# Kernel tuning notes

Hardware: AMD Instinct MI355X
Metric: run time of the kernel (lower is better)

Reference implementation:

```python
import jax, jax.numpy as jnp
import numpy as np

N = 50000      # nodes
E = 800000     # edges (avg degree 16)
NE = 100000    # query edges
IN = 128; HID = 128; OUT = 128; FEAT = 2


def _linear_params(k, fan_in, fan_out):
    # torch.nn.Linear default init: U(-1/sqrt(fan_in), 1/sqrt(fan_in))
    s = 1.0 / np.sqrt(fan_in)
    k1, k2 = jax.random.split(k)
    W = jax.random.uniform(k1, (fan_in, fan_out), jnp.float32, -s, s)
    b = jax.random.uniform(k2, (fan_out,), jnp.float32, -s, s)
    return W, b


def setup_inputs() -> dict:
    key = jax.random.key(0)
    ks = jax.random.split(key, 9)
    inp = {}
    inp["x"] = jax.random.normal(ks[0], (N, IN), jnp.float32)
    inp["adj_t"] = jax.random.randint(ks[1], (2, E), 0, N)          # edge_index [2,E]
    inp["train_edges"] = jax.random.randint(ks[2], (NE, 2), 0, N)   # query edges
    # GCNConv stack params (lin weight + bias per layer)
    inp["W1"], inp["b1"] = _linear_params(ks[3], IN, HID)
    inp["W2"], inp["b2"] = _linear_params(ks[4], HID, HID)
    inp["W3"], inp["b3"] = _linear_params(ks[5], HID, OUT)
    # LinkPredictor MLP params
    inp["P1"], inp["pb1"] = _linear_params(ks[6], OUT, HID)
    inp["P2"], inp["pb2"] = _linear_params(ks[7], HID, HID)
    inp["P3"], inp["pb3"] = _linear_params(ks[8], HID, FEAT)
    return inp


def gcn_conv(x, edge_index, W, b):
    # GCNConv(normalize=False), edge_weight=None:
    #   h = x @ W; out[dst] += h[src]; out += bias
    h = x @ W                                    # [N, d_out]
    msg = h[edge_index[0]]                       # gather  [E, d_out]
    out = jax.ops.segment_sum(msg, edge_index[1], num_segments=x.shape[0])
    return out + b


def reference(x, adj_t, train_edges, W1, b1, W2, b2, W3, b3, P1, pb1, P2, pb2, P3, pb3):
    # GCN trunk (eval mode -> dropout is identity; dropout=0 anyway)
    h = jax.nn.relu(gcn_conv(x, adj_t, W1, b1))
    h = jax.nn.relu(gcn_conv(h, adj_t, W2, b2))
    emb = gcn_conv(h, adj_t, W3, b3)             # [N, OUT]
    # LinkPredictor on (src, dst) node-embedding pairs
    z = emb[train_edges[:, 0]] * emb[train_edges[:, 1]]   # [NE, OUT]
    z = jax.nn.relu(z @ P1 + pb1)
    z = jax.nn.relu(z @ P2 + pb2)
    z = z @ P3 + pb3                                       # [NE, FEAT]
    # F.normalize(p=2, dim=-1) with eps=1e-12
    z = z / jnp.maximum(jnp.linalg.norm(z, axis=-1, keepdims=True), 1e-12)
    pred = jax.nn.log_softmax(z, axis=-1)
    return pred[None]                                      # torch.unsqueeze(pred, 0)
```

## Files before the change

kernel.cpp:

```cpp
#include <hip/hip_runtime.h>
#include <math.h>

#define N_NODES 50000
#define N_EDGES 800000
#define N_QE    100000
#define D       128

typedef _Float16 half8 __attribute__((ext_vector_type(8)));
typedef short    short8 __attribute__((ext_vector_type(8)));
typedef float    f32x4 __attribute__((ext_vector_type(4)));

static __device__ inline short f2bf(float f) {
    unsigned u = __builtin_bit_cast(unsigned, f);
    u += 0x7FFFu + ((u >> 16) & 1u);
    return (short)(u >> 16);
}

static const size_t O_CNT = 0;
static const size_t O_OFF = 256u * 1024;
static const size_t O_CUR = 512u * 1024;
static const size_t O_BS  = 768u * 1024;
static const size_t O_SRC = 1024u * 1024;
static const size_t O_G   = 8u << 20;
static const size_t O_H   = O_G + 12800000u;
static const size_t O_T   = O_H + 12800000u;

__global__ void k_count(const int* __restrict__ dst, int* __restrict__ cnt) {
    int e = blockIdx.x * 256 + threadIdx.x;
    if (e < N_EDGES) atomicAdd(&cnt[dst[e]], 1);
}

__global__ __launch_bounds__(256)
void k_scan1(const int* __restrict__ cnt, int* __restrict__ off,
             int* __restrict__ bsum) {
    __shared__ int sh[256];
    const int t = threadIdx.x;
    const int i = blockIdx.x * 256 + t;
    int v = (i < N_NODES) ? cnt[i] : 0;
    sh[t] = v;
    __syncthreads();
    #pragma unroll
    for (int o = 1; o < 256; o <<= 1) {
        int u = (t >= o) ? sh[t - o] : 0;
        __syncthreads();
        sh[t] += u;
        __syncthreads();
    }
    if (i < N_NODES) off[i] = sh[t] - v;
    if (t == 255) bsum[blockIdx.x] = sh[255];
}

__global__ __launch_bounds__(256)
void k_scan2(int* __restrict__ bsum, int nblk) {
    __shared__ int sh[256];
    const int t = threadIdx.x;
    int v = (t < nblk) ? bsum[t] : 0;
    sh[t] = v;
    __syncthreads();
    #pragma unroll
    for (int o = 1; o < 256; o <<= 1) {
        int u = (t >= o) ? sh[t - o] : 0;
        __syncthreads();
        sh[t] += u;
        __syncthreads();
    }
    if (t < nblk) bsum[t] = sh[t] - v;
}

__global__ __launch_bounds__(256)
void k_scan3(int* __restrict__ off, const int* __restrict__ bsum,
             int* __restrict__ cur) {
    const int i = blockIdx.x * 256 + threadIdx.x;
    if (i < N_NODES) {
        int o = off[i] + bsum[blockIdx.x];
        off[i] = o;
        cur[i] = o;
    }
    if (i == 0) off[N_NODES] = N_EDGES;
}

__global__ void k_scatter(const int* __restrict__ src, const int* __restrict__ dst,
                          int* __restrict__ cur, int* __restrict__ srcs) {
    int e = blockIdx.x * 256 + threadIdx.x;
    if (e < N_EDGES) {
        int p = atomicAdd(&cur[dst[e]], 1);
        srcs[p] = src[e];
    }
}

__global__ __launch_bounds__(256)
void k_t16all(const float* __restrict__ W1, const float* __restrict__ W2,
              const float* __restrict__ W3, const float* __restrict__ Q1,
              const float* __restrict__ Q2, short* __restrict__ T)
{
    int m = blockIdx.x >> 6;
    const float* S = (m == 0) ? W1 : (m == 1) ? W2 : (m == 2) ? W3
                   : (m == 3) ? Q1 : Q2;
    short* Dp = T + m * 16384;
    int idx = (blockIdx.x & 63) * 256 + threadIdx.x;
    int c = idx & 127, k = idx >> 7;
    Dp[c * 128 + k] = f2bf(S[k * 128 + c]);
}


template<typename XT>
__global__ __launch_bounds__(256)
void k_mm(const XT* __restrict__ X, const short* __restrict__ WT,
          _Float16* __restrict__ Y, int rows)
{
    __shared__ __align__(16) short xs[64 * 128];
    const int tid = threadIdx.x;
    const int l   = tid & 63;
    const int w   = tid >> 6;
    const int g   = l >> 4;
    const int l15 = l & 15;
    const int row0 = blockIdx.x * 64;

    {
        int r = tid >> 2;
        int gr = row0 + r; if (gr >= rows) gr = rows - 1;
        const XT* src = X + (size_t)gr * D;
        #pragma unroll
        for (int it = 0; it < 4; ++it) {
            int s = (tid & 3) + it * 4;
            short8 h;
            if constexpr (sizeof(XT) == 4) {
                float4 v0 = *(const float4*)((const float*)src + s * 8);
                float4 v1 = *(const float4*)((const float*)src + s * 8 + 4);
                h[0] = f2bf(v0.x); h[1] = f2bf(v0.y);
                h[2] = f2bf(v0.z); h[3] = f2bf(v0.w);
                h[4] = f2bf(v1.x); h[5] = f2bf(v1.y);
                h[6] = f2bf(v1.z); h[7] = f2bf(v1.w);
            } else {
                half8 v = *(const half8*)((const _Float16*)src + s * 8);
                #pragma unroll
                for (int c = 0; c < 8; ++c) h[c] = f2bf((float)v[c]);
            }
            *(short8*)&xs[r * 128 + ((s ^ (r & 7)) * 8)] = h;
        }
    }

    short8 wf[2][4];
    #pragma unroll
    for (int tt = 0; tt < 2; ++tt) {
        int c = w * 32 + tt * 16 + l15;
        #pragma unroll
        for (int s = 0; s < 4; ++s)
            wf[tt][s] = *(const short8*)(WT + (size_t)c * 128 + s * 32 + g * 8);
    }

    __syncthreads();

    f32x4 acc[4][2];
    #pragma unroll
    for (int rt = 0; rt < 4; ++rt)
        #pragma unroll
        for (int tt = 0; tt < 2; ++tt)
            acc[rt][tt] = (f32x4){0.f, 0.f, 0.f, 0.f};

    #pragma unroll
    for (int rt = 0; rt < 4; ++rt) {
        const int r = rt * 16 + l15;
        short8 a[4];
        #pragma unroll
        for (int s = 0; s < 4; ++s) {
            int slot = (4 * s + g) ^ (r & 7);
            a[s] = *(const short8*)&xs[r * 128 + slot * 8];
        }
        #pragma unroll
        for (int tt = 0; tt < 2; ++tt)
            #pragma unroll
            for (int s = 0; s < 4; ++s)
                acc[rt][tt] = __builtin_amdgcn_mfma_f32_16x16x32_bf16(
                    a[s], wf[tt][s], acc[rt][tt], 0, 0, 0);
    }

    __syncthreads();

    #pragma unroll
    for (int rt = 0; rt < 4; ++rt)
        #pragma unroll
        for (int tt = 0; tt < 2; ++tt) {
            int c = w * 32 + tt * 16 + l15;
            #pragma unroll
            for (int i = 0; i < 4; ++i) {
                int row = rt * 16 + g * 4 + i;
                int slot = (c >> 3) ^ (row & 7);
                xs[row * 128 + slot * 8 + (c & 7)] =
                    (short)__builtin_bit_cast(unsigned short, (_Float16)acc[rt][tt][i]);
            }
        }
    __syncthreads();

    {
        int r = tid >> 2;
        int gr = row0 + r;
        if (gr < rows) {
            short* dstp = (short*)(Y + (size_t)gr * D);
            #pragma unroll
            for (int it = 0; it < 4; ++it) {
                int s = (tid & 3) + it * 4;
                *(short8*)(dstp + s * 8) =
                    *(const short8*)&xs[r * 128 + ((s ^ (r & 7)) * 8)];
            }
        }
    }
}

template<bool RELU>
__global__ __launch_bounds__(256)
void k_agg(const _Float16* __restrict__ Hin, const int* __restrict__ off,
           const int* __restrict__ srcs, const float* __restrict__ bias,
           _Float16* __restrict__ Hout)
{
    const int lane = threadIdx.x & 63;
    const int es   = lane >> 4;
    const int q    = lane & 15;
    const int wv   = threadIdx.x >> 6;
    const int n    = blockIdx.x * 4 + wv;
    const int j0 = __builtin_amdgcn_readfirstlane(off[n]);
    const int j1 = __builtin_amdgcn_readfirstlane(off[n + 1]);

    float acc[8] = {};
    int j = j0;

    for (; j + 16 <= j1; j += 16) {
        half8 v[4];
        #pragma unroll
        for (int k = 0; k < 4; ++k) {
            int s = srcs[j + 4 * k + es];
            v[k] = *(const half8*)(Hin + (size_t)s * D + q * 8);
        }
        #pragma unroll
        for (int k = 0; k < 4; ++k)
            #pragma unroll
            for (int c = 0; c < 8; ++c) acc[c] += (float)v[k][c];
    }
    for (; j + 4 <= j1; j += 4) {
        int s = srcs[j + es];
        half8 v = *(const half8*)(Hin + (size_t)s * D + q * 8);
        #pragma unroll
        for (int c = 0; c < 8; ++c) acc[c] += (float)v[c];
    }
    {
        int rem = j1 - j;
        if (rem > 0) {
            int s = srcs[j + (es < rem ? es : rem - 1)];
            half8 v = *(const half8*)(Hin + (size_t)s * D + q * 8);
            if (es < rem) {
                #pragma unroll
                for (int c = 0; c < 8; ++c) acc[c] += (float)v[c];
            }
        }
    }

    #pragma unroll
    for (int c = 0; c < 8; ++c) {
        acc[c] += __shfl_xor(acc[c], 16, 64);
        acc[c] += __shfl_xor(acc[c], 32, 64);
    }

    if (es == 0) {
        half8 o;
        #pragma unroll
        for (int c = 0; c < 8; ++c) {
            float t = acc[c] + bias[q * 8 + c];
            if (RELU) t = fmaxf(t, 0.f);
            o[c] = (_Float16)t;
        }
        *(half8*)(Hout + (size_t)n * D + q * 8) = o;
    }
}

__global__ __launch_bounds__(256)
void k_predm(const _Float16* __restrict__ emb, const int* __restrict__ te,
             const short* __restrict__ P1T, const float* __restrict__ pb1,
             const short* __restrict__ P2T, const float* __restrict__ pb2,
             const float* __restrict__ P3, const float* __restrict__ pb3,
             float* __restrict__ out)
{
    __shared__ __align__(16) short xs[64 * 128];
    __shared__ float red[64][8];
    const int tid = threadIdx.x;
    const int l   = tid & 63;
    const int w   = tid >> 6;
    const int g   = l >> 4;
    const int l15 = l & 15;
    const int row0 = blockIdx.x * 64;

    {
        int r = tid >> 2;
        int e = row0 + r; if (e >= N_QE) e = N_QE - 1;
        const int2 ee = *(const int2*)(te + 2 * e);
        const _Float16* sp = emb + (size_t)ee.x * D;
        const _Float16* dp = emb + (size_t)ee.y * D;
        #pragma unroll
        for (int it = 0; it < 4; ++it) {
            int s = (tid & 3) + it * 4;
            half8 a = *(const half8*)(sp + s * 8);
            half8 b = *(const half8*)(dp + s * 8);
            short8 h;
            #pragma unroll
            for (int c = 0; c < 8; ++c) h[c] = f2bf((float)a[c] * (float)b[c]);
            *(short8*)&xs[r * 128 + ((s ^ (r & 7)) * 8)] = h;
        }
    }
    __syncthreads();

    f32x4 acc[4][2];

    {
        short8 wf[2][4];
        #pragma unroll
        for (int tt = 0; tt < 2; ++tt) {
            int c = w * 32 + tt * 16 + l15;
            #pragma unroll
            for (int s = 0; s < 4; ++s)
                wf[tt][s] = *(const short8*)(P1T + (size_t)c * 128 + s * 32 + g * 8);
        }
        #pragma unroll
        for (int rt = 0; rt < 4; ++rt)
            #pragma unroll
            for (int tt = 0; tt < 2; ++tt)
                acc[rt][tt] = (f32x4){0.f, 0.f, 0.f, 0.f};

        #pragma unroll
        for (int rt = 0; rt < 4; ++rt) {
            const int r = rt * 16 + l15;
            short8 a[4];
            #pragma unroll
            for (int s = 0; s < 4; ++s) {
                int slot = (4 * s + g) ^ (r & 7);
                a[s] = *(const short8*)&xs[r * 128 + slot * 8];
            }
            #pragma unroll
            for (int tt = 0; tt < 2; ++tt)
                #pragma unroll
                for (int s = 0; s < 4; ++s)
                    acc[rt][tt] = __builtin_amdgcn_mfma_f32_16x16x32_bf16(
                        a[s], wf[tt][s], acc[rt][tt], 0, 0, 0);
        }

        float bv[2];
        #pragma unroll
        for (int tt = 0; tt < 2; ++tt) bv[tt] = pb1[w * 32 + tt * 16 + l15];

        __syncthreads();

        #pragma unroll
        for (int rt = 0; rt < 4; ++rt)
            #pragma unroll
            for (int tt = 0; tt < 2; ++tt) {
                int c = w * 32 + tt * 16 + l15;
                #pragma unroll
                for (int i = 0; i < 4; ++i) {
                    float v = fmaxf(acc[rt][tt][i] + bv[tt], 0.f);
                    int row = rt * 16 + g * 4 + i;
                    int slot = (c >> 3) ^ (row & 7);
                    xs[row * 128 + slot * 8 + (c & 7)] = f2bf(v);
                }
            }
        __syncthreads();
    }

    {
        short8 wf[2][4];
        #pragma unroll
        for (int tt = 0; tt < 2; ++tt) {
            int c = w * 32 + tt * 16 + l15;
            #pragma unroll
            for (int s = 0; s < 4; ++s)
                wf[tt][s] = *(const short8*)(P2T + (size_t)c * 128 + s * 32 + g * 8);
        }
        #pragma unroll
        for (int rt = 0; rt < 4; ++rt)
            #pragma unroll
            for (int tt = 0; tt < 2; ++tt)
                acc[rt][tt] = (f32x4){0.f, 0.f, 0.f, 0.f};

        #pragma unroll
        for (int rt = 0; rt < 4; ++rt) {
            const int r = rt * 16 + l15;
            short8 a[4];
            #pragma unroll
            for (int s = 0; s < 4; ++s) {
                int slot = (4 * s + g) ^ (r & 7);
                a[s] = *(const short8*)&xs[r * 128 + slot * 8];
            }
            #pragma unroll
            for (int tt = 0; tt < 2; ++tt)
                #pragma unroll
                for (int s = 0; s < 4; ++s)
                    acc[rt][tt] = __builtin_amdgcn_mfma_f32_16x16x32_bf16(
                        a[s], wf[tt][s], acc[rt][tt], 0, 0, 0);
        }
    }

    {
        float bv[2];
        float2 p3v[2];
        #pragma unroll
        for (int tt = 0; tt < 2; ++tt) {
            int c = w * 32 + tt * 16 + l15;
            bv[tt] = pb2[c];
            p3v[tt] = *(const float2*)(P3 + c * 2);
        }
        #pragma unroll
        for (int rt = 0; rt < 4; ++rt)
            #pragma unroll
            for (int i = 0; i < 4; ++i) {
                float z0 = fmaxf(acc[rt][0][i] + bv[0], 0.f);
                float z1 = fmaxf(acc[rt][1][i] + bv[1], 0.f);
                float p0 = z0 * p3v[0].x + z1 * p3v[1].x;
                float p1 = z0 * p3v[0].y + z1 * p3v[1].y;
                #pragma unroll
                for (int o = 1; o < 16; o <<= 1) {
                    p0 += __shfl_xor(p0, o, 64);
                    p1 += __shfl_xor(p1, o, 64);
                }
                if (l15 == 0) {
                    int row = rt * 16 + g * 4 + i;
                    red[row][w * 2]     = p0;
                    red[row][w * 2 + 1] = p1;
                }
            }
    }
    __syncthreads();

    if (tid < 64) {
        int gr = row0 + tid;
        if (gr < N_QE) {
            float p0 = red[tid][0] + red[tid][2] + red[tid][4] + red[tid][6] + pb3[0];
            float p1 = red[tid][1] + red[tid][3] + red[tid][5] + red[tid][7] + pb3[1];
            float nrm = fmaxf(sqrtf(p0 * p0 + p1 * p1), 1e-12f);
            p0 /= nrm; p1 /= nrm;
            float m = fmaxf(p0, p1);
            float lse = m + logf(expf(p0 - m) + expf(p1 - m));
            out[gr * 2]     = p0 - lse;
            out[gr * 2 + 1] = p1 - lse;
        }
    }
}

extern "C" void kernel_launch(void* const* d_in, const int* in_sizes, int n_in,
                              void* d_out, int out_size, void* d_ws, size_t ws_size,
                              hipStream_t stream)
{
    (void)in_sizes; (void)n_in; (void)out_size; (void)ws_size;
    const float* x   = (const float*)d_in[0];
    const int*   adj = (const int*)d_in[1];
    const int*   te  = (const int*)d_in[2];
    const float* W1  = (const float*)d_in[3];
    const float* b1  = (const float*)d_in[4];
    const float* W2  = (const float*)d_in[5];
    const float* b2  = (const float*)d_in[6];
    const float* W3  = (const float*)d_in[7];
    const float* b3  = (const float*)d_in[8];
    const float* P1  = (const float*)d_in[9];
    const float* pb1 = (const float*)d_in[10];
    const float* P2  = (const float*)d_in[11];
    const float* pb2 = (const float*)d_in[12];
    const float* P3  = (const float*)d_in[13];
    const float* pb3 = (const float*)d_in[14];
    float* out = (float*)d_out;

    char* ws = (char*)d_ws;
    int* cnt  = (int*)(ws + O_CNT);
    int* off  = (int*)(ws + O_OFF);
    int* cur  = (int*)(ws + O_CUR);
    int* bsum = (int*)(ws + O_BS);
    int* srcs = (int*)(ws + O_SRC);
    _Float16* G = (_Float16*)(ws + O_G);
    _Float16* H = (_Float16*)(ws + O_H);
    short*    T = (short*)(ws + O_T);

    const int* esrc = adj;
    const int* edst = adj + N_EDGES;

    const int SBLK = (N_NODES + 255) / 256;

    k_t16all<<<320, 256, 0, stream>>>(W1, W2, W3, P1, P2, T);

    hipMemsetAsync(cnt, 0, N_NODES * sizeof(int), stream);
    k_count<<<N_EDGES / 256, 256, 0, stream>>>(edst, cnt);
    k_scan1<<<SBLK, 256, 0, stream>>>(cnt, off, bsum);
    k_scan2<<<1, 256, 0, stream>>>(bsum, SBLK);
    k_scan3<<<SBLK, 256, 0, stream>>>(off, bsum, cur);
    k_scatter<<<N_EDGES / 256, 256, 0, stream>>>(esrc, edst, cur, srcs);

    const int gN = (N_NODES + 63) / 64;

    k_mm<float><<<gN, 256, 0, stream>>>(x, T, H, N_NODES);
    k_agg<true><<<N_NODES / 4, 256, 0, stream>>>(H, off, srcs, b1, G);
    k_mm<_Float16><<<gN, 256, 0, stream>>>(G, T + 16384, H, N_NODES);
    k_agg<true><<<N_NODES / 4, 256, 0, stream>>>(H, off, srcs, b2, G);
    k_mm<_Float16><<<gN, 256, 0, stream>>>(G, T + 2 * 16384, H, N_NODES);
    k_agg<false><<<N_NODES / 4, 256, 0, stream>>>(H, off, srcs, b3, G);

    const int gQ = (N_QE + 63) / 64;
    k_predm<<<gQ, 256, 0, stream>>>(G, te, T + 3 * 16384, pb1,
                                    T + 4 * 16384, pb2, P3, pb3, out);
}
```

Baseline: 345.0 us.

## Build CSR with two-pass bucketed partition and 16-bit source indices

```diff
diff --git a/kernel.cpp b/kernel.cpp
--- a/kernel.cpp
+++ b/kernel.cpp
@@ -5,6 +5,8 @@
 #define N_EDGES 800000
 #define N_QE    100000
 #define D       128
+#define NB      391
+#define PCHUNK  8192
 
 typedef _Float16 half8 __attribute__((ext_vector_type(8)));
 typedef short    short8 __attribute__((ext_vector_type(8)));
@@ -18,9 +20,10 @@
 
 static const size_t O_CNT = 0;
 static const size_t O_OFF = 256u * 1024;
-static const size_t O_CUR = 512u * 1024;
+static const size_t O_BC  = 512u * 1024;
 static const size_t O_BS  = 768u * 1024;
 static const size_t O_SRC = 1024u * 1024;
+static const size_t O_TMP = 4u << 20;
 static const size_t O_G   = 8u << 20;
 static const size_t O_H   = O_G + 12800000u;
 static const size_t O_T   = O_H + 12800000u;
@@ -68,23 +71,64 @@
 }
 
 __global__ __launch_bounds__(256)
-void k_scan3(int* __restrict__ off, const int* __restrict__ bsum,
-             int* __restrict__ cur) {
+void k_scan3(int* __restrict__ off, const int* __restrict__ bsum) {
     const int i = blockIdx.x * 256 + threadIdx.x;
-    if (i < N_NODES) {
-        int o = off[i] + bsum[blockIdx.x];
-        off[i] = o;
-        cur[i] = o;
-    }
+    if (i < N_NODES) off[i] = off[i] + bsum[blockIdx.x];
     if (i == 0) off[N_NODES] = N_EDGES;
 }
 
-__global__ void k_scatter(const int* __restrict__ src, const int* __restrict__ dst,
-                          int* __restrict__ cur, int* __restrict__ srcs) {
-    int e = blockIdx.x * 256 + threadIdx.x;
-    if (e < N_EDGES) {
-        int p = atomicAdd(&cur[dst[e]], 1);
-        srcs[p] = src[e];
+__global__ void k_binit(const int* __restrict__ off, int* __restrict__ bcur) {
+    int b = blockIdx.x * 256 + threadIdx.x;
+    if (b < NB) bcur[b] = off[b << 7];
+}
+
+__global__ __launch_bounds__(256)
+void k_part(const int* __restrict__ src, const int* __restrict__ dst,
+            int* __restrict__ bcur, unsigned* __restrict__ tmp)
+{
+    __shared__ int hcnt[NB];
+    __shared__ int lpos[NB];
+    __shared__ int base[NB];
+    const int t = threadIdx.x;
+    const int e0 = blockIdx.x * PCHUNK;
+    const int e1 = (e0 + PCHUNK < N_EDGES) ? e0 + PCHUNK : N_EDGES;
+
+    for (int b = t; b < NB; b += 256) { hcnt[b] = 0; lpos[b] = 0; }
+    __syncthreads();
+    for (int e = e0 + t; e < e1; e += 256)
+        atomicAdd(&hcnt[dst[e] >> 7], 1);
+    __syncthreads();
+    for (int b = t; b < NB; b += 256) {
+        int c = hcnt[b];
+        base[b] = c ? atomicAdd(&bcur[b], c) : 0;
+    }
+    __syncthreads();
+    for (int e = e0 + t; e < e1; e += 256) {
+        int d = dst[e];
+        int b = d >> 7;
+        int pos = atomicAdd(&lpos[b], 1);
+        tmp[base[b] + pos] = (unsigned)src[e] | ((unsigned)(d & 127) << 16);
+    }
+}
+
+__global__ __launch_bounds__(256)
+void k_fine(const unsigned* __restrict__ tmp, const int* __restrict__ off,
+            unsigned short* __restrict__ srcs)
+{
+    __shared__ int fcur[129];
+    const int t = threadIdx.x;
+    const int b = blockIdx.x;
+    const int n0 = b << 7;
+    const int nn = (N_NODES - n0 < 128) ? N_NODES - n0 : 128;
+    if (t <= nn) fcur[t] = off[n0 + t];
+    const int r0 = off[n0];
+    const int r1 = off[n0 + nn];
+    __syncthreads();
+    for (int i = r0 + t; i < r1; i += 256) {
+        unsigned en = tmp[i];
+        int dl = en >> 16;
+        int p = atomicAdd(&fcur[dl], 1);
+        srcs[p] = (unsigned short)(en & 0xFFFFu);
     }
 }
 
@@ -210,7 +254,7 @@
 template<bool RELU>
 __global__ __launch_bounds__(256)
 void k_agg(const _Float16* __restrict__ Hin, const int* __restrict__ off,
-           const int* __restrict__ srcs, const float* __restrict__ bias,
+           const unsigned short* __restrict__ srcs, const float* __restrict__ bias,
            _Float16* __restrict__ Hout)
 {
     const int lane = threadIdx.x & 63;
@@ -467,9 +511,10 @@
     char* ws = (char*)d_ws;
     int* cnt  = (int*)(ws + O_CNT);
     int* off  = (int*)(ws + O_OFF);
-    int* cur  = (int*)(ws + O_CUR);
+    int* bcur = (int*)(ws + O_BC);
     int* bsum = (int*)(ws + O_BS);
-    int* srcs = (int*)(ws + O_SRC);
+    unsigned short* srcs = (unsigned short*)(ws + O_SRC);
+    unsigned* tmp = (unsigned*)(ws + O_TMP);
     _Float16* G = (_Float16*)(ws + O_G);
     _Float16* H = (_Float16*)(ws + O_H);
     short*    T = (short*)(ws + O_T);
@@ -485,8 +530,10 @@
     k_count<<<N_EDGES / 256, 256, 0, stream>>>(edst, cnt);
     k_scan1<<<SBLK, 256, 0, stream>>>(cnt, off, bsum);
     k_scan2<<<1, 256, 0, stream>>>(bsum, SBLK);
-    k_scan3<<<SBLK, 256, 0, stream>>>(off, bsum, cur);
-    k_scatter<<<N_EDGES / 256, 256, 0, stream>>>(esrc, edst, cur, srcs);
+    k_scan3<<<SBLK, 256, 0, stream>>>(off, bsum);
+    k_binit<<<2, 256, 0, stream>>>(off, bcur);
+    k_part<<<(N_EDGES + PCHUNK - 1) / PCHUNK, 256, 0, stream>>>(esrc, edst, bcur, tmp);
+    k_fine<<<NB, 256, 0, stream>>>(tmp, off, srcs);
 
     const int gN = (N_NODES + 63) / 64;
 
```

Result: faster. 331.1 us (-4.0%).
